# Kernel optimization log

Hardware: AMD Instinct MI355X
Metric: run time of the kernel (lower is better)

The kernel has to match this reference:

```python
import jax, jax.numpy as jnp
import numpy as np

IDIM = 1024
HIDDEN = 4096
N_EXPERT = 8
T = 2048


def setup_inputs() -> dict:
    key = jax.random.key(0)
    ks = jax.random.split(key, 6)
    s_in = 1.0 / np.sqrt(IDIM)
    s_h = 1.0 / np.sqrt(HIDDEN)
    return {
        "xs": jax.random.normal(ks[0], (T, IDIM), dtype=jnp.float32),
        "top_k": 2,
        # gate: Linear(idim -> n_expert, bias=False); torch weight (E, D)
        "Wg": jax.random.uniform(ks[1], (N_EXPERT, IDIM), jnp.float32, -s_in, s_in),
        # experts stacked: w_1 Linear(idim->hidden), w_2 Linear(hidden->idim)
        "W1": jax.random.uniform(ks[2], (N_EXPERT, IDIM, HIDDEN), jnp.float32, -s_in, s_in),
        "b1": jax.random.uniform(ks[3], (N_EXPERT, HIDDEN), jnp.float32, -s_in, s_in),
        "W2": jax.random.uniform(ks[4], (N_EXPERT, HIDDEN, IDIM), jnp.float32, -s_h, s_h),
        "b2": jax.random.uniform(ks[5], (N_EXPERT, IDIM), jnp.float32, -s_h, s_h),
    }


def reference(xs, top_k, Wg, W1, b1, W2, b2):
    # Router: (T, E)
    router = xs @ Wg.T
    logits, selected = jax.lax.top_k(router, top_k)          # (T, k)
    # softmax over the top-k slot axis in fp32, cast back (matches torch)
    weights = jax.nn.softmax(logits.astype(jnp.float32), axis=-1).astype(xs.dtype)
    # combine weight per token per expert: (T, E). Tokens not routed to an
    # expert get weight 0, zeroing that expert's contribution (same math as
    # the masked gather / scatter-add in the torch loop).
    onehot = jax.nn.one_hot(selected, N_EXPERT, dtype=xs.dtype)  # (T, k, E)
    comb = jnp.einsum("tk,tke->te", weights, onehot)
    # all-expert FFN (dropout_rate = 0 -> identity)
    h = jax.nn.relu(jnp.einsum("td,edh->teh", xs, W1) + b1[None, :, :])
    y = jnp.einsum("teh,ehd->ted", h, W2) + b2[None, :, :]
    return jnp.einsum("te,ted->td", comb, y)
```

## Files before the change

### kernel.cpp

```cpp
#include <hip/hip_runtime.h>
#include <stdint.h>

#define T_TOK 2048
#define IDIM  1024
#define HID   4096
#define NE    8
#define BM    128
#define BN    128
#define BN2   64
#define BK    64
#define RMAX  5120
#define MAXTILES 40

typedef __bf16 bf16;
typedef bf16  bf16x8 __attribute__((ext_vector_type(8)));
typedef float f32x4  __attribute__((ext_vector_type(4)));

#define WS_NTILES   128
#define WS_TILE_E   192
#define WS_TILE_R   448
#define WS_TOK_E    1024
#define WS_TOK_W    17408
#define WS_ROW_TOK  33792
#define WS_ROW_W    54272
#define XG_OFF      131072

__global__ __launch_bounds__(256) void k_zero_out(float4* __restrict__ a) {
    a[blockIdx.x * 256 + threadIdx.x] = make_float4(0.f, 0.f, 0.f, 0.f);
}

__global__ __launch_bounds__(256) void k_router(const float* __restrict__ xs,
                                                const float* __restrict__ Wg,
                                                int* __restrict__ tok_e,
                                                float* __restrict__ tok_w) {
    __shared__ float sWg[NE * IDIM];
    for (int i = threadIdx.x; i < NE * IDIM; i += 256) sWg[i] = Wg[i];
    __syncthreads();
    int wave = threadIdx.x >> 6, lane = threadIdx.x & 63;
    int t = blockIdx.x * 4 + wave;
    if (t >= T_TOK) return;
    float p[NE];
#pragma unroll
    for (int e = 0; e < NE; e++) p[e] = 0.f;
    for (int j = 0; j < IDIM / 64; j++) {
        float x = xs[(size_t)t * IDIM + j * 64 + lane];
#pragma unroll
        for (int e = 0; e < NE; e++)
            p[e] += x * sWg[e * IDIM + j * 64 + lane];
    }
#pragma unroll
    for (int e = 0; e < NE; e++) {
        float v = p[e];
        for (int off = 32; off > 0; off >>= 1) v += __shfl_down(v, off);
        p[e] = v;
    }
    if (lane == 0) {
        int e0 = 0; float l0 = p[0];
        for (int e = 1; e < NE; e++) if (p[e] > l0) { l0 = p[e]; e0 = e; }
        int e1 = -1; float l1 = -1e30f;
        for (int e = 0; e < NE; e++) if (e != e0 && p[e] > l1) { l1 = p[e]; e1 = e; }
        if (e1 < 0) e1 = (e0 + 1) & 7;
        float z = __expf(l1 - l0);
        tok_e[2 * t]     = e0;  tok_e[2 * t + 1] = e1;
        tok_w[2 * t]     = 1.f / (1.f + z);
        tok_w[2 * t + 1] = z / (1.f + z);
    }
}

__global__ __launch_bounds__(256) void k_setup(int* __restrict__ w,
                                               float* __restrict__ wf) {
    __shared__ int cnt[NE];
    __shared__ int cur[NE];
    int tid = threadIdx.x;
    if (tid < NE) cnt[tid] = 0;
    for (int i = tid; i < RMAX; i += 256) w[WS_ROW_TOK / 4 + i] = -1;
    __syncthreads();
    for (int i = tid; i < 2 * T_TOK; i += 256)
        atomicAdd(&cnt[w[WS_TOK_E / 4 + i]], 1);
    __syncthreads();
    if (tid == 0) {
        int off = 0, nt = 0;
        for (int e = 0; e < NE; e++) {
            cur[e] = off;
            int nb = (cnt[e] + BM - 1) / BM;
            for (int b = 0; b < nb && nt < MAXTILES; b++) {
                w[WS_TILE_E / 4 + nt] = e;
                w[WS_TILE_R / 4 + nt] = off + b * BM;
                nt++;
            }
            off += nb * BM;
        }
        w[WS_NTILES / 4] = nt;
    }
    __syncthreads();
    for (int i = tid; i < 2 * T_TOK; i += 256) {
        int e   = w[WS_TOK_E / 4 + i];
        int pos = atomicAdd(&cur[e], 1);
        if (pos < RMAX) {
            w[WS_ROW_TOK / 4 + pos] = i >> 1;
            wf[WS_ROW_W / 4 + pos]  = wf[WS_TOK_W / 4 + i];
        }
    }
}

__device__ inline uint4 pack8(float4 a, float4 b) {
    union { bf16 h[8]; uint4 u; } pk;
    pk.h[0] = (bf16)a.x; pk.h[1] = (bf16)a.y; pk.h[2] = (bf16)a.z; pk.h[3] = (bf16)a.w;
    pk.h[4] = (bf16)b.x; pk.h[5] = (bf16)b.y; pk.h[6] = (bf16)b.z; pk.h[7] = (bf16)b.w;
    return pk.u;
}
__device__ inline uint32_t pack2(float a, float b) {
    union { bf16 h[2]; uint32_t u; } pk;
    pk.h[0] = (bf16)a; pk.h[1] = (bf16)b;
    return pk.u;
}

__device__ __forceinline__ void g2l16(const bf16* g, bf16* l) {
    __builtin_amdgcn_global_load_lds(
        (const __attribute__((address_space(1))) void*)g,
        (__attribute__((address_space(3))) void*)l, 16, 0, 0);
}

__global__ __launch_bounds__(256) void k_gather(const float* __restrict__ xs,
                                                const int* __restrict__ wsi,
                                                bf16* __restrict__ Xg) {
    int wv = threadIdx.x >> 6, lane = threadIdx.x & 63;
    int r = blockIdx.x * 4 + wv;
    int tok = wsi[WS_ROW_TOK / 4 + r];
#pragma unroll
    for (int i = 0; i < 2; i++) {
        int c = i * 64 + lane;
        uint4 v;
        if (tok >= 0) {
            const float* g = xs + (size_t)tok * IDIM + c * 8;
            v = pack8(*(const float4*)g, *(const float4*)(g + 4));
        } else v = make_uint4(0u, 0u, 0u, 0u);
        int cs = (c & ~7) | ((c & 7) ^ (r & 7));
        *(uint4*)&Xg[(size_t)r * IDIM + cs * 8] = v;
    }
}

__global__ __launch_bounds__(256) void k_cvt(const float* __restrict__ src,
                                             bf16* __restrict__ dst,
                                             int ld_src, int k0, int n0, int KL,
                                             size_t s_estride, size_t d_estride) {
    __shared__ bf16 sT[64 * 66];
    int e = blockIdx.y;
    const float* S = src + (size_t)e * s_estride;
    bf16* D = dst + (size_t)e * d_estride;
    int ntk = KL >> 6;
    int tk = blockIdx.x % ntk, tn = blockIdx.x / ntk;
    int t = threadIdx.x;
#pragma unroll
    for (int i = 0; i < 4; i++) {
        int idx = t + i * 256;
        int k = idx >> 4, n4 = (idx & 15) * 4;
        float4 v = *(const float4*)&S[(size_t)(k0 + tk * 64 + k) * ld_src +
                                      n0 + tn * 64 + n4];
        *(uint32_t*)&sT[k * 66 + n4]     = pack2(v.x, v.y);
        *(uint32_t*)&sT[k * 66 + n4 + 2] = pack2(v.z, v.w);
    }
    __syncthreads();
#pragma unroll
    for (int j = 0; j < 2; j++) {
        int idx = t + j * 256;
        int n = idx >> 3, kq = idx & 7;
        union { bf16 h[8]; uint4 u; } pk;
#pragma unroll
        for (int jj = 0; jj < 8; jj++) pk.h[jj] = sT[(kq * 8 + jj) * 66 + n];
        int ng = tn * 64 + n;
        int ch = kq ^ (ng & 7);
        *(uint4*)&D[(size_t)ng * KL + tk * 64 + ch * 8] = pk.u;
    }
}

__global__ __launch_bounds__(256) void k_ffn1n(const bf16* __restrict__ Xg,
                                               const bf16* __restrict__ W1t,
                                               const float* __restrict__ b1,
                                               const int* __restrict__ wsi,
                                               bf16* __restrict__ H,
                                               int h0, int CW) {
    int tile = blockIdx.y;
    if (tile >= wsi[WS_NTILES / 4]) return;
    int e    = wsi[WS_TILE_E / 4 + tile];
    int row0 = wsi[WS_TILE_R / 4 + tile];
    int n0   = blockIdx.x * BN;

    const bf16* Abase = Xg + (size_t)row0 * IDIM;
    const bf16* Bbase = W1t + ((size_t)e * CW + n0) * IDIM;

    __shared__ bf16 sA[BM * BK];
    __shared__ bf16 sB[BN * BK];

    int t = threadIdx.x, lane = t & 63;
    int wv = t >> 6, wx = wv & 1, wy = wv >> 1;
    int lm = lane & 15, q = lane >> 4;

    f32x4 acc[4][4];
#pragma unroll
    for (int i = 0; i < 4; i++)
#pragma unroll
        for (int j = 0; j < 4; j++) acc[i][j] = (f32x4){0.f, 0.f, 0.f, 0.f};

    for (int kc = 0; kc < IDIM / BK; kc++) {
        if (kc) __syncthreads();
#pragma unroll
        for (int i = 0; i < 4; i++) {
            int s = t + i * 256;
            g2l16(Abase + (size_t)(s >> 3) * IDIM + kc * BK + (s & 7) * 8,
                  &sA[s * 8]);
        }
#pragma unroll
        for (int i = 0; i < 4; i++) {
            int s = t + i * 256;
            g2l16(Bbase + (size_t)(s >> 3) * IDIM + kc * BK + (s & 7) * 8,
                  &sB[s * 8]);
        }
        __syncthreads();
#pragma unroll
        for (int ks = 0; ks < 2; ks++) {
            bf16x8 aF[4], bF[4];
#pragma unroll
            for (int mt = 0; mt < 4; mt++) {
                int r = wy * 64 + mt * 16 + lm;
                aF[mt] = *(const bf16x8*)&sA[r * BK + (((ks * 4 + q) ^ (r & 7)) * 8)];
            }
#pragma unroll
            for (int nt = 0; nt < 4; nt++) {
                int r = wx * 64 + nt * 16 + lm;
                bF[nt] = *(const bf16x8*)&sB[r * BK + (((ks * 4 + q) ^ (r & 7)) * 8)];
            }
#pragma unroll
            for (int mt = 0; mt < 4; mt++)
#pragma unroll
                for (int nt = 0; nt < 4; nt++)
                    acc[mt][nt] = __builtin_amdgcn_mfma_f32_16x16x32_bf16(
                        aF[mt], bF[nt], acc[mt][nt], 0, 0, 0);
        }
    }
#pragma unroll
    for (int nt = 0; nt < 4; nt++) {
        int col = n0 + wx * 64 + nt * 16 + lm;
        float bv = b1[(size_t)e * HID + h0 + col];
#pragma unroll
        for (int mt = 0; mt < 4; mt++) {
#pragma unroll
            for (int r = 0; r < 4; r++) {
                int rg = row0 + wy * 64 + mt * 16 + q * 4 + r;
                float v = fmaxf(acc[mt][nt][r] + bv, 0.f);
                int sc = (col & ~63) | ((col & 63) ^ ((rg & 7) << 3));
                H[(size_t)rg * CW + sc] = (bf16)v;
            }
        }
    }
}

__global__ __launch_bounds__(256) void k_ffn2n(const bf16* __restrict__ H,
                                               const bf16* __restrict__ W2t,
                                               const float* __restrict__ b2,
                                               const int* __restrict__ wsi,
                                               const float* __restrict__ wsf,
                                               float* __restrict__ out,
                                               int CW, int addb) {
    int tile = blockIdx.y;
    if (tile >= wsi[WS_NTILES / 4]) return;
    int e    = wsi[WS_TILE_E / 4 + tile];
    int row0 = wsi[WS_TILE_R / 4 + tile];
    int n0   = blockIdx.x * BN2;

    const int*   row_tok = wsi + WS_ROW_TOK / 4;
    const float* row_w   = wsf + WS_ROW_W / 4;
    const bf16* Abase = H + (size_t)row0 * CW;
    const bf16* Bbase = W2t + ((size_t)e * IDIM + n0) * CW;

    __shared__ bf16 sA[BM * BK];
    __shared__ bf16 sB[BN2 * BK];

    int t = threadIdx.x, lane = t & 63;
    int wv = t >> 6, wx = wv & 1, wy = wv >> 1;
    int lm = lane & 15, q = lane >> 4;

    f32x4 acc[4][2];
#pragma unroll
    for (int i = 0; i < 4; i++)
#pragma unroll
        for (int j = 0; j < 2; j++) acc[i][j] = (f32x4){0.f, 0.f, 0.f, 0.f};

    for (int kc = 0; kc < CW / BK; kc++) {
        if (kc) __syncthreads();
#pragma unroll
        for (int i = 0; i < 4; i++) {
            int s = t + i * 256;
            g2l16(Abase + (size_t)(s >> 3) * CW + kc * BK + (s & 7) * 8,
                  &sA[s * 8]);
        }
#pragma unroll
        for (int i = 0; i < 2; i++) {
            int s = t + i * 256;
            g2l16(Bbase + (size_t)(s >> 3) * CW + kc * BK + (s & 7) * 8,
                  &sB[s * 8]);
        }
        __syncthreads();
#pragma unroll
        for (int ks = 0; ks < 2; ks++) {
            bf16x8 aF[4], bF[2];
#pragma unroll
            for (int mt = 0; mt < 4; mt++) {
                int r = wy * 64 + mt * 16 + lm;
                aF[mt] = *(const bf16x8*)&sA[r * BK + (((ks * 4 + q) ^ (r & 7)) * 8)];
            }
#pragma unroll
            for (int nt = 0; nt < 2; nt++) {
                int r = wx * 32 + nt * 16 + lm;
                bF[nt] = *(const bf16x8*)&sB[r * BK + (((ks * 4 + q) ^ (r & 7)) * 8)];
            }
#pragma unroll
            for (int mt = 0; mt < 4; mt++)
#pragma unroll
                for (int nt = 0; nt < 2; nt++)
                    acc[mt][nt] = __builtin_amdgcn_mfma_f32_16x16x32_bf16(
                        aF[mt], bF[nt], acc[mt][nt], 0, 0, 0);
        }
    }

    int   tokr[16];
    float wr[16];
#pragma unroll
    for (int mt = 0; mt < 4; mt++)
#pragma unroll
        for (int r = 0; r < 4; r++) {
            int rg = row0 + wy * 64 + mt * 16 + q * 4 + r;
            tokr[mt * 4 + r] = row_tok[rg];
            wr[mt * 4 + r]   = row_w[rg];
        }
#pragma unroll
    for (int nt = 0; nt < 2; nt++) {
        int col  = n0 + wx * 32 + nt * 16 + lm;
        float bv = addb ? b2[(size_t)e * IDIM + col] : 0.f;
#pragma unroll
        for (int mt = 0; mt < 4; mt++)
#pragma unroll
            for (int r = 0; r < 4; r++) {
                int tok = tokr[mt * 4 + r];
                if (tok >= 0)
                    atomicAdd(&out[(size_t)tok * IDIM + col],
                              wr[mt * 4 + r] * (acc[mt][nt][r] + bv));
            }
    }
}

__global__ __launch_bounds__(256) void k_fallback(const float* __restrict__ xs,
                                                  const float* __restrict__ Wg,
                                                  const float* __restrict__ W1,
                                                  const float* __restrict__ b1,
                                                  const float* __restrict__ W2,
                                                  const float* __restrict__ b2,
                                                  float* __restrict__ out) {
    __shared__ float xbuf[IDIM];
    __shared__ float hbuf[256];
    __shared__ float slog[NE];
    __shared__ int   sel[2];
    __shared__ float selw[2];

    int t   = blockIdx.x;
    int tid = threadIdx.x;

    for (int i = tid; i < IDIM; i += 256)
        xbuf[i] = xs[(size_t)t * IDIM + i];
    __syncthreads();
    {
        int e = tid >> 5, l = tid & 31;
        float p = 0.f;
        for (int d = l; d < IDIM; d += 32)
            p += xbuf[d] * Wg[e * IDIM + d];
        for (int off = 16; off > 0; off >>= 1) p += __shfl_down(p, off, 32);
        if (l == 0) slog[e] = p;
    }
    __syncthreads();
    if (tid == 0) {
        int e0 = 0; float l0 = slog[0];
        for (int e = 1; e < NE; e++) if (slog[e] > l0) { l0 = slog[e]; e0 = e; }
        int e1 = -1; float l1 = -1e30f;
        for (int e = 0; e < NE; e++) if (e != e0 && slog[e] > l1) { l1 = slog[e]; e1 = e; }
        if (e1 < 0) e1 = (e0 + 1) & 7;
        float z = __expf(l1 - l0);
        sel[0] = e0; sel[1] = e1;
        selw[0] = 1.f / (1.f + z);
        selw[1] = z / (1.f + z);
    }
    __syncthreads();

    float ytot[4] = {0.f, 0.f, 0.f, 0.f};
#pragma unroll
    for (int s = 0; s < 2; s++) {
        int   e = sel[s];
        float w = selw[s];
        const float* W1e = W1 + (size_t)e * IDIM * HID;
        const float* W2e = W2 + (size_t)e * HID * IDIM;
        float ys[4] = {0.f, 0.f, 0.f, 0.f};
        for (int hb = 0; hb < HID / 256; hb++) {
            int h = hb * 256 + tid;
            float acc = b1[e * HID + h];
            for (int d = 0; d < IDIM; d++)
                acc += xbuf[d] * W1e[(size_t)d * HID + h];
            __syncthreads();
            hbuf[tid] = fmaxf(acc, 0.f);
            __syncthreads();
            for (int hh = 0; hh < 256; hh++) {
                float hv = hbuf[hh];
                const float* wrow = W2e + (size_t)(hb * 256 + hh) * IDIM;
#pragma unroll
                for (int cc = 0; cc < 4; cc++)
                    ys[cc] += hv * wrow[cc * 256 + tid];
            }
        }
#pragma unroll
        for (int cc = 0; cc < 4; cc++)
            ytot[cc] += w * (ys[cc] + b2[e * IDIM + cc * 256 + tid]);
    }
#pragma unroll
    for (int cc = 0; cc < 4; cc++)
        out[(size_t)t * IDIM + cc * 256 + tid] = ytot[cc];
}

extern "C" void kernel_launch(void* const* d_in, const int* in_sizes, int n_in,
                              void* d_out, int out_size, void* d_ws, size_t ws_size,
                              hipStream_t stream) {
    int o = (n_in >= 7 && in_sizes[1] == 1) ? 1 : 0;
    const float* xs = (const float*)d_in[0];
    const float* Wg = (const float*)d_in[1 + o];
    const float* W1 = (const float*)d_in[2 + o];
    const float* b1 = (const float*)d_in[3 + o];
    const float* W2 = (const float*)d_in[4 + o];
    const float* b2 = (const float*)d_in[5 + o];
    float* out = (float*)d_out;

    size_t xg_sz = (size_t)RMAX * IDIM * 2;
    int CW = 0;
    if (d_ws) {
        for (int c = HID; c >= 512; c >>= 1) {
            size_t need = (size_t)XG_OFF + xg_sz + (size_t)RMAX * c * 2 +
                          (size_t)NE * c * IDIM * 2;
            if (ws_size >= need) { CW = c; break; }
        }
    }
    if (!CW) {
        k_fallback<<<T_TOK, 256, 0, stream>>>(xs, Wg, W1, b1, W2, b2, out);
        return;
    }

    char*  ws  = (char*)d_ws;
    int*   wsi = (int*)d_ws;
    float* wsf = (float*)d_ws;
    bf16*  Xg  = (bf16*)(ws + XG_OFF);
    bf16*  Hb  = (bf16*)(ws + XG_OFF + xg_sz);
    bf16*  Wt  = (bf16*)(ws + XG_OFF + xg_sz + (size_t)RMAX * CW * 2);

    k_zero_out<<<T_TOK, 256, 0, stream>>>((float4*)out);
    k_router<<<T_TOK / 4, 256, 0, stream>>>(xs, Wg, wsi + WS_TOK_E / 4,
                                            wsf + WS_TOK_W / 4);
    k_setup<<<1, 256, 0, stream>>>(wsi, wsf);
    k_gather<<<RMAX / 4, 256, 0, stream>>>(xs, wsi, Xg);

    int HC = HID / CW;
    for (int c = 0; c < HC; c++) {
        k_cvt<<<dim3((IDIM / 64) * (CW / 64), NE), 256, 0, stream>>>(
            W1, Wt, HID, 0, c * CW, IDIM,
            (size_t)IDIM * HID, (size_t)CW * IDIM);
        k_ffn1n<<<dim3(CW / BN, MAXTILES), 256, 0, stream>>>(
            Xg, Wt, b1, wsi, Hb, c * CW, CW);
        k_cvt<<<dim3((CW / 64) * (IDIM / 64), NE), 256, 0, stream>>>(
            W2, Wt, IDIM, c * CW, 0, CW,
            (size_t)HID * IDIM, (size_t)IDIM * CW);
        k_ffn2n<<<dim3(IDIM / BN2, MAXTILES), 256, 0, stream>>>(
            Hb, Wt, b2, wsi, wsf, out, CW, c == 0 ? 1 : 0);
    }
}
```

Before: 441.7 us.

## Split-K the second FFN GEMM, widen its N tile, and remap blocks across XCDs

The second expert GEMM now uses 128-wide N tiles instead of 64 and splits the K (hidden) dimension across a third grid axis of up to 4 slices. Partial results are merged through the atomicAdd epilogue that already existed, and only slice 0 adds the bias. Both FFN kernels remap block IDs so that consecutive logical tiles land on the same XCD, aiming for better L2 reuse of shared weight and activation tiles. The split-K multiplies the atomic traffic to the output, and the wider tile raises register pressure.

```diff
diff --git a/kernel.cpp b/kernel.cpp
--- a/kernel.cpp
+++ b/kernel.cpp
@@ -7,7 +7,6 @@
 #define NE    8
 #define BM    128
 #define BN    128
-#define BN2   64
 #define BK    64
 #define RMAX  5120
 #define MAXTILES 40
@@ -24,6 +23,12 @@
 #define WS_ROW_TOK  33792
 #define WS_ROW_W    54272
 #define XG_OFF      131072
+
+__device__ __forceinline__ int xcd_remap(int orig, int nwg) {
+    int q = nwg >> 3, r = nwg & 7;
+    int xcd = orig & 7, idx = orig >> 3;
+    return (xcd < r ? xcd * (q + 1) : r * (q + 1) + (xcd - r) * q) + idx;
+}
 
 __global__ __launch_bounds__(256) void k_zero_out(float4* __restrict__ a) {
     a[blockIdx.x * 256 + threadIdx.x] = make_float4(0.f, 0.f, 0.f, 0.f);
@@ -180,11 +185,14 @@
                                                const int* __restrict__ wsi,
                                                bf16* __restrict__ H,
                                                int h0, int CW) {
-    int tile = blockIdx.y;
+    int gx = gridDim.x;
+    int orig = blockIdx.x + gx * blockIdx.y;
+    int wgid = xcd_remap(orig, gx * gridDim.y);
+    int bx = wgid % gx, tile = wgid / gx;
     if (tile >= wsi[WS_NTILES / 4]) return;
     int e    = wsi[WS_TILE_E / 4 + tile];
     int row0 = wsi[WS_TILE_R / 4 + tile];
-    int n0   = blockIdx.x * BN;
+    int n0   = bx * BN;
 
     const bf16* Abase = Xg + (size_t)row0 * IDIM;
     const bf16* Bbase = W1t + ((size_t)e * CW + n0) * IDIM;
@@ -262,31 +270,38 @@
                                                const float* __restrict__ wsf,
                                                float* __restrict__ out,
                                                int CW, int addb) {
-    int tile = blockIdx.y;
+    int gx = gridDim.x, gy = gridDim.y;
+    int orig = blockIdx.x + gx * (blockIdx.y + gy * blockIdx.z);
+    int wgid = xcd_remap(orig, gx * gy * (int)gridDim.z);
+    int bx   = wgid % gx;
+    int tile = (wgid / gx) % gy;
+    int bz   = wgid / (gx * gy);
     if (tile >= wsi[WS_NTILES / 4]) return;
     int e    = wsi[WS_TILE_E / 4 + tile];
     int row0 = wsi[WS_TILE_R / 4 + tile];
-    int n0   = blockIdx.x * BN2;
+    int n0   = bx * BN;
+    int kw   = CW / gridDim.z;
+    int kb   = bz * kw;
 
     const int*   row_tok = wsi + WS_ROW_TOK / 4;
     const float* row_w   = wsf + WS_ROW_W / 4;
-    const bf16* Abase = H + (size_t)row0 * CW;
-    const bf16* Bbase = W2t + ((size_t)e * IDIM + n0) * CW;
+    const bf16* Abase = H + (size_t)row0 * CW + kb;
+    const bf16* Bbase = W2t + ((size_t)e * IDIM + n0) * CW + kb;
 
     __shared__ bf16 sA[BM * BK];
-    __shared__ bf16 sB[BN2 * BK];
+    __shared__ bf16 sB[BN * BK];
 
     int t = threadIdx.x, lane = t & 63;
     int wv = t >> 6, wx = wv & 1, wy = wv >> 1;
     int lm = lane & 15, q = lane >> 4;
 
-    f32x4 acc[4][2];
+    f32x4 acc[4][4];
 #pragma unroll
     for (int i = 0; i < 4; i++)
 #pragma unroll
-        for (int j = 0; j < 2; j++) acc[i][j] = (f32x4){0.f, 0.f, 0.f, 0.f};
-
-    for (int kc = 0; kc < CW / BK; kc++) {
+        for (int j = 0; j < 4; j++) acc[i][j] = (f32x4){0.f, 0.f, 0.f, 0.f};
+
+    for (int kc = 0; kc < kw / BK; kc++) {
         if (kc) __syncthreads();
 #pragma unroll
         for (int i = 0; i < 4; i++) {
@@ -295,7 +310,7 @@
                   &sA[s * 8]);
         }
 #pragma unroll
-        for (int i = 0; i < 2; i++) {
+        for (int i = 0; i < 4; i++) {
             int s = t + i * 256;
             g2l16(Bbase + (size_t)(s >> 3) * CW + kc * BK + (s & 7) * 8,
                   &sB[s * 8]);
@@ -303,21 +318,21 @@
         __syncthreads();
 #pragma unroll
         for (int ks = 0; ks < 2; ks++) {
-            bf16x8 aF[4], bF[2];
+            bf16x8 aF[4], bF[4];
 #pragma unroll
             for (int mt = 0; mt < 4; mt++) {
                 int r = wy * 64 + mt * 16 + lm;
                 aF[mt] = *(const bf16x8*)&sA[r * BK + (((ks * 4 + q) ^ (r & 7)) * 8)];
             }
 #pragma unroll
-            for (int nt = 0; nt < 2; nt++) {
-                int r = wx * 32 + nt * 16 + lm;
+            for (int nt = 0; nt < 4; nt++) {
+                int r = wx * 64 + nt * 16 + lm;
                 bF[nt] = *(const bf16x8*)&sB[r * BK + (((ks * 4 + q) ^ (r & 7)) * 8)];
             }
 #pragma unroll
             for (int mt = 0; mt < 4; mt++)
 #pragma unroll
-                for (int nt = 0; nt < 2; nt++)
+                for (int nt = 0; nt < 4; nt++)
                     acc[mt][nt] = __builtin_amdgcn_mfma_f32_16x16x32_bf16(
                         aF[mt], bF[nt], acc[mt][nt], 0, 0, 0);
         }
@@ -333,10 +348,11 @@
             tokr[mt * 4 + r] = row_tok[rg];
             wr[mt * 4 + r]   = row_w[rg];
         }
-#pragma unroll
-    for (int nt = 0; nt < 2; nt++) {
-        int col  = n0 + wx * 32 + nt * 16 + lm;
-        float bv = addb ? b2[(size_t)e * IDIM + col] : 0.f;
+    int dobias = addb && (bz == 0);
+#pragma unroll
+    for (int nt = 0; nt < 4; nt++) {
+        int col  = n0 + wx * 64 + nt * 16 + lm;
+        float bv = dobias ? b2[(size_t)e * IDIM + col] : 0.f;
 #pragma unroll
         for (int mt = 0; mt < 4; mt++)
 #pragma unroll
@@ -462,6 +478,9 @@
     k_setup<<<1, 256, 0, stream>>>(wsi, wsf);
     k_gather<<<RMAX / 4, 256, 0, stream>>>(xs, wsi, Xg);
 
+    int SK = 4;
+    while (CW / SK < BK) SK >>= 1;
+
     int HC = HID / CW;
     for (int c = 0; c < HC; c++) {
         k_cvt<<<dim3((IDIM / 64) * (CW / 64), NE), 256, 0, stream>>>(
@@ -472,7 +491,7 @@
         k_cvt<<<dim3((CW / 64) * (IDIM / 64), NE), 256, 0, stream>>>(
             W2, Wt, IDIM, c * CW, 0, CW,
             (size_t)HID * IDIM, (size_t)IDIM * CW);
-        k_ffn2n<<<dim3(IDIM / BN2, MAXTILES), 256, 0, stream>>>(
+        k_ffn2n<<<dim3(IDIM / BN, MAXTILES, SK), 256, 0, stream>>>(
             Hb, Wt, b2, wsi, wsf, out, CW, c == 0 ? 1 : 0);
     }
 }
```

Result: slower. 511.1 us (+15.7%).

## Replace atomic scatter-add with per-row Y buffer and combine kernel; remap blocks per XCD

Applied to the files above, without the earlier changes.

The second FFN GEMM now writes unweighted expert outputs into a per-row fp32 buffer Y with plain stores instead of atomically adding weighted results into the output. A new combine kernel gathers each token's two rows and applies the routing weights, which also removes the output zeroing kernel. Both GEMM kernels also remap workgroup ids so consecutive tiles land on the same XCD, aiming for better L2 reuse. This adds an extra fp32 buffer write and read in exchange for removing scattered atomics, and it needs more workspace, which may push the chunk-width choice lower.

```diff
diff --git a/kernel.cpp b/kernel.cpp
--- a/kernel.cpp
+++ b/kernel.cpp
@@ -23,10 +23,13 @@
 #define WS_TOK_W    17408
 #define WS_ROW_TOK  33792
 #define WS_ROW_W    54272
+#define WS_TOK_POS  74752
 #define XG_OFF      131072
 
-__global__ __launch_bounds__(256) void k_zero_out(float4* __restrict__ a) {
-    a[blockIdx.x * 256 + threadIdx.x] = make_float4(0.f, 0.f, 0.f, 0.f);
+__device__ __forceinline__ int xcd_remap(int orig, int nwg) {
+    int q = nwg >> 3, r = nwg & 7;
+    int xcd = orig & 7, idx = orig >> 3;
+    return (xcd < r ? xcd * (q + 1) : r * (q + 1) + (xcd - r) * q) + idx;
 }
 
 __global__ __launch_bounds__(256) void k_router(const float* __restrict__ xs,
@@ -99,6 +102,9 @@
         if (pos < RMAX) {
             w[WS_ROW_TOK / 4 + pos] = i >> 1;
             wf[WS_ROW_W / 4 + pos]  = wf[WS_TOK_W / 4 + i];
+            w[WS_TOK_POS / 4 + i]   = pos;
+        } else {
+            w[WS_TOK_POS / 4 + i]   = 0;
         }
     }
 }
@@ -180,11 +186,14 @@
                                                const int* __restrict__ wsi,
                                                bf16* __restrict__ H,
                                                int h0, int CW) {
-    int tile = blockIdx.y;
+    int gx = gridDim.x;
+    int orig = blockIdx.x + gx * blockIdx.y;
+    int wgid = xcd_remap(orig, gx * gridDim.y);
+    int bx = wgid % gx, tile = wgid / gx;
     if (tile >= wsi[WS_NTILES / 4]) return;
     int e    = wsi[WS_TILE_E / 4 + tile];
     int row0 = wsi[WS_TILE_R / 4 + tile];
-    int n0   = blockIdx.x * BN;
+    int n0   = bx * BN;
 
     const bf16* Abase = Xg + (size_t)row0 * IDIM;
     const bf16* Bbase = W1t + ((size_t)e * CW + n0) * IDIM;
@@ -255,21 +264,21 @@
     }
 }
 
-__global__ __launch_bounds__(256) void k_ffn2n(const bf16* __restrict__ H,
+__global__ __launch_bounds__(256) void k_ffn2y(const bf16* __restrict__ H,
                                                const bf16* __restrict__ W2t,
                                                const float* __restrict__ b2,
                                                const int* __restrict__ wsi,
-                                               const float* __restrict__ wsf,
-                                               float* __restrict__ out,
-                                               int CW, int addb) {
-    int tile = blockIdx.y;
+                                               float* __restrict__ Y,
+                                               int CW, int first) {
+    int gx = gridDim.x;
+    int orig = blockIdx.x + gx * blockIdx.y;
+    int wgid = xcd_remap(orig, gx * gridDim.y);
+    int bx = wgid % gx, tile = wgid / gx;
     if (tile >= wsi[WS_NTILES / 4]) return;
     int e    = wsi[WS_TILE_E / 4 + tile];
     int row0 = wsi[WS_TILE_R / 4 + tile];
-    int n0   = blockIdx.x * BN2;
-
-    const int*   row_tok = wsi + WS_ROW_TOK / 4;
-    const float* row_w   = wsf + WS_ROW_W / 4;
+    int n0   = bx * BN2;
+
     const bf16* Abase = H + (size_t)row0 * CW;
     const bf16* Bbase = W2t + ((size_t)e * IDIM + n0) * CW;
 
@@ -323,30 +332,41 @@
         }
     }
 
-    int   tokr[16];
-    float wr[16];
-#pragma unroll
-    for (int mt = 0; mt < 4; mt++)
-#pragma unroll
-        for (int r = 0; r < 4; r++) {
-            int rg = row0 + wy * 64 + mt * 16 + q * 4 + r;
-            tokr[mt * 4 + r] = row_tok[rg];
-            wr[mt * 4 + r]   = row_w[rg];
-        }
 #pragma unroll
     for (int nt = 0; nt < 2; nt++) {
         int col  = n0 + wx * 32 + nt * 16 + lm;
-        float bv = addb ? b2[(size_t)e * IDIM + col] : 0.f;
+        float bv = first ? b2[(size_t)e * IDIM + col] : 0.f;
 #pragma unroll
         for (int mt = 0; mt < 4; mt++)
 #pragma unroll
             for (int r = 0; r < 4; r++) {
-                int tok = tokr[mt * 4 + r];
-                if (tok >= 0)
-                    atomicAdd(&out[(size_t)tok * IDIM + col],
-                              wr[mt * 4 + r] * (acc[mt][nt][r] + bv));
-            }
-    }
+                int rg = row0 + wy * 64 + mt * 16 + q * 4 + r;
+                float* p = &Y[(size_t)rg * IDIM + col];
+                float v  = acc[mt][nt][r] + bv;
+                *p = first ? v : (*p + v);
+            }
+    }
+}
+
+__global__ __launch_bounds__(256) void k_combine(const float* __restrict__ Y,
+                                                 const int* __restrict__ wsi,
+                                                 const float* __restrict__ wsf,
+                                                 float* __restrict__ out) {
+    int tok = blockIdx.x;
+    int p0 = wsi[WS_TOK_POS / 4 + 2 * tok];
+    int p1 = wsi[WS_TOK_POS / 4 + 2 * tok + 1];
+    float w0 = wsf[WS_TOK_W / 4 + 2 * tok];
+    float w1 = wsf[WS_TOK_W / 4 + 2 * tok + 1];
+    int c = threadIdx.x;
+    const float4* y0 = (const float4*)(Y + (size_t)p0 * IDIM);
+    const float4* y1 = (const float4*)(Y + (size_t)p1 * IDIM);
+    float4 a = y0[c], b = y1[c];
+    float4 r;
+    r.x = w0 * a.x + w1 * b.x;
+    r.y = w0 * a.y + w1 * b.y;
+    r.z = w0 * a.z + w1 * b.z;
+    r.w = w0 * a.w + w1 * b.w;
+    ((float4*)(out + (size_t)tok * IDIM))[c] = r;
 }
 
 __global__ __launch_bounds__(256) void k_fallback(const float* __restrict__ xs,
@@ -436,11 +456,12 @@
     float* out = (float*)d_out;
 
     size_t xg_sz = (size_t)RMAX * IDIM * 2;
+    size_t y_sz  = (size_t)RMAX * IDIM * 4;
     int CW = 0;
     if (d_ws) {
         for (int c = HID; c >= 512; c >>= 1) {
             size_t need = (size_t)XG_OFF + xg_sz + (size_t)RMAX * c * 2 +
-                          (size_t)NE * c * IDIM * 2;
+                          (size_t)NE * c * IDIM * 2 + y_sz;
             if (ws_size >= need) { CW = c; break; }
         }
     }
@@ -455,8 +476,9 @@
     bf16*  Xg  = (bf16*)(ws + XG_OFF);
     bf16*  Hb  = (bf16*)(ws + XG_OFF + xg_sz);
     bf16*  Wt  = (bf16*)(ws + XG_OFF + xg_sz + (size_t)RMAX * CW * 2);
-
-    k_zero_out<<<T_TOK, 256, 0, stream>>>((float4*)out);
+    float* Yb  = (float*)(ws + XG_OFF + xg_sz + (size_t)RMAX * CW * 2 +
+                          (size_t)NE * CW * IDIM * 2);
+
     k_router<<<T_TOK / 4, 256, 0, stream>>>(xs, Wg, wsi + WS_TOK_E / 4,
                                             wsf + WS_TOK_W / 4);
     k_setup<<<1, 256, 0, stream>>>(wsi, wsf);
@@ -472,7 +494,8 @@
         k_cvt<<<dim3((CW / 64) * (IDIM / 64), NE), 256, 0, stream>>>(
             W2, Wt, IDIM, c * CW, 0, CW,
             (size_t)HID * IDIM, (size_t)IDIM * CW);
-        k_ffn2n<<<dim3(IDIM / BN2, MAXTILES), 256, 0, stream>>>(
-            Hb, Wt, b2, wsi, wsf, out, CW, c == 0 ? 1 : 0);
-    }
-}
+        k_ffn2y<<<dim3(IDIM / BN2, MAXTILES), 256, 0, stream>>>(
+            Hb, Wt, b2, wsi, Yb, CW, c == 0 ? 1 : 0);
+    }
+    k_combine<<<T_TOK, 256, 0, stream>>>(Yb, wsi, wsf, out);
+}
```

Measured after the change: 438.5 us. About the same (-0.7%).
